# Optimization experiments

Hardware: AMD Instinct MI355X
Metric: run time of the kernel (lower is better)

Reference implementation:

```python
import jax, jax.numpy as jnp
import numpy as np

N_GROUPS = 32
EPS = 1e-5
N_HEADS = 8
D_K = 64


def setup_inputs() -> dict:
    key = jax.random.key(0)
    ks = jax.random.split(key, 4)
    B, C, H, W = 16, 512, 32, 32
    x = jax.random.normal(ks[0], (B, C, H, W), dtype=jnp.float32)
    gn_w = jnp.ones((C,), dtype=jnp.float32)
    gn_b = jnp.zeros((C,), dtype=jnp.float32)
    proj_w = jax.random.normal(ks[1], (3 * C, C), dtype=jnp.float32) * (C ** -0.5)
    proj_b = jnp.zeros((3 * C,), dtype=jnp.float32)
    out_w = jax.random.normal(ks[2], (C, C), dtype=jnp.float32) * (C ** -0.5)
    out_b = jnp.zeros((C,), dtype=jnp.float32)
    return {"x": x, "gn_w": gn_w, "gn_b": gn_b, "proj_w": proj_w,
            "proj_b": proj_b, "out_w": out_w, "out_b": out_b}


def _group_norm(x, w, b):
    B, C, H, W = x.shape
    xg = x.reshape(B, N_GROUPS, C // N_GROUPS, H, W)
    mean = xg.mean(axis=(2, 3, 4), keepdims=True)
    var = xg.var(axis=(2, 3, 4), keepdims=True)
    xn = (xg - mean) * jax.lax.rsqrt(var + EPS)
    xn = xn.reshape(B, C, H, W)
    return xn * w[None, :, None, None] + b[None, :, None, None]


def reference(x, gn_w, gn_b, proj_w, proj_b, out_w, out_b):
    B, C, H, W = x.shape
    S = H * W
    scale = D_K ** -0.25  # applied to both q and k, as in the original
    h = _group_norm(x, gn_w, gn_b).reshape(B, C, S).transpose(0, 2, 1)  # [B,S,C]
    qkv = h @ proj_w.T + proj_b  # [B,S,3C]
    qkv = qkv.reshape(B, S, N_HEADS, 3 * D_K)
    q, k, v = jnp.split(qkv, 3, axis=-1)  # each [B,S,H,D]
    attn = jnp.einsum('bihd,bjhd->bijh', q * scale, k * scale)  # [B,S,S,Hd]
    attn = jax.nn.softmax(attn, axis=2)
    res = jnp.einsum('bijh,bjhd->bihd', attn, v).reshape(B, S, N_HEADS * D_K)
    res = res @ out_w.T + out_b  # [B,S,C]
    res = res.transpose(0, 2, 1).reshape(B, C, H, W)
    return res + x
```

## Files before the change

### kernel.cpp

```cpp
#include <hip/hip_runtime.h>
#include <stdint.h>

typedef unsigned short u16;
typedef __attribute__((ext_vector_type(8))) short bf16x8;
typedef __attribute__((ext_vector_type(4))) short bf16x4;
typedef __attribute__((ext_vector_type(4))) float f32x4;
typedef __attribute__((ext_vector_type(4))) unsigned short u16x4;

#define GLD16(gp, lp) __builtin_amdgcn_global_load_lds( \
    (__attribute__((address_space(1))) void*)(void*)(gp), \
    (__attribute__((address_space(3))) void*)(void*)(lp), 16, 0, 0)

__device__ __forceinline__ u16 f2b(float f) {
  union { float f; unsigned u; } v; v.f = f;
  unsigned r = v.u + 0x7FFFu + ((v.u >> 16) & 1u);
  return (u16)(r >> 16);
}

__device__ __forceinline__ float fexp2(float x) {
#if __has_builtin(__builtin_amdgcn_exp2f)
  return __builtin_amdgcn_exp2f(x);
#else
  return exp2f(x);
#endif
}

__global__ __launch_bounds__(256) void cvt_kernel(const float* __restrict__ wq_f,
                                                  const float* __restrict__ wo_f,
                                                  u16* __restrict__ wq,
                                                  u16* __restrict__ wo) {
  int i = blockIdx.x * 256 + threadIdx.x;
  const float* src; u16* dst; int j;
  if (i < 196608) { src = wq_f; dst = wq; j = i; }
  else            { src = wo_f; dst = wo; j = i - 196608; }
  const float4 f = ((const float4*)src)[j];
  u16x4 r; r[0] = f2b(f.x); r[1] = f2b(f.y); r[2] = f2b(f.z); r[3] = f2b(f.w);
  *(u16x4*)(dst + (size_t)j * 4) = r;
}

__global__ __launch_bounds__(256) void gn_kernel(const float* __restrict__ x,
                                                 const float* __restrict__ gw,
                                                 const float* __restrict__ gb,
                                                 u16* __restrict__ h) {
  const int b = blockIdx.x >> 5, g = blockIdx.x & 31;
  const float* xg = x + ((size_t)(b * 512 + g * 16)) * 1024;
  const int tid = threadIdx.x;
  float vals[64];
  float s = 0.f, ss = 0.f;
#pragma unroll
  for (int i = 0; i < 64; i++) {
    float vv = xg[i * 256 + tid];
    vals[i] = vv; s += vv; ss += vv * vv;
  }
#pragma unroll
  for (int off = 32; off; off >>= 1) { s += __shfl_down(s, off); ss += __shfl_down(ss, off); }
  __shared__ float red[8];
  const int wid = tid >> 6, lane = tid & 63;
  if (lane == 0) { red[wid] = s; red[4 + wid] = ss; }
  __syncthreads();
  if (tid == 0) {
    float S = red[0] + red[1] + red[2] + red[3];
    float SS = red[4] + red[5] + red[6] + red[7];
    float mean = S * (1.f / 16384.f);
    float var = SS * (1.f / 16384.f) - mean * mean;
    red[0] = mean; red[1] = rsqrtf(var + 1e-5f);
  }
  __syncthreads();
  const float mean = red[0], rs = red[1];
  float sc[16], bi[16];
#pragma unroll
  for (int c = 0; c < 16; c++) { sc[c] = gw[g * 16 + c] * rs; bi[c] = gb[g * 16 + c]; }
#pragma unroll
  for (int h4 = 0; h4 < 4; h4++) {
    const int sp = h4 * 256 + tid;
    u16 row[16];
#pragma unroll
    for (int c = 0; c < 16; c++)
      row[c] = f2b((vals[c * 4 + h4] - mean) * sc[c] + bi[c]);
    u16* dst = h + ((size_t)(b * 1024 + sp)) * 512 + g * 16;
    *(bf16x8*)dst = *(bf16x8*)&row[0];
    *(bf16x8*)(dst + 8) = *(bf16x8*)&row[8];
  }
}

__global__ __launch_bounds__(256) void qkv_gemm(const u16* __restrict__ h,
                                                const u16* __restrict__ w,
                                                const float* __restrict__ bias,
                                                u16* __restrict__ q,
                                                u16* __restrict__ k,
                                                u16* __restrict__ v) {
  __shared__ u16 As[128 * 32];
  __shared__ u16 Bs[128 * 32];
  const int b = blockIdx.z;
  const int bm = blockIdx.x;
  const int bn = blockIdx.y;
  const int tid = threadIdx.x, lane = tid & 63, wid = tid >> 6;
  const int wm = wid & 1, wn = wid >> 1;
  const u16* gA = h + ((size_t)b * 1024 + bm * 128) * 512;
  const u16* gB = w + (size_t)bn * 128 * 512;

  const f32x4 fz = {0.f, 0.f, 0.f, 0.f};
  f32x4 acc[4][4];
#pragma unroll
  for (int i = 0; i < 4; i++)
#pragma unroll
    for (int j = 0; j < 4; j++) acc[i][j] = fz;

  const int r0 = lane >> 2;
  const int ch8 = (lane & 3) * 8;

  for (int kt = 0; kt < 16; ++kt) {
    __syncthreads();
#pragma unroll
    for (int j = 0; j < 2; ++j) {
      const int idx = wid * 2 + j;
      const int row = idx * 16 + r0;
      GLD16(gA + (size_t)row * 512 + kt * 32 + ch8, &As[idx * 512 + lane * 8]);
      GLD16(gB + (size_t)row * 512 + kt * 32 + ch8, &Bs[idx * 512 + lane * 8]);
    }
    __syncthreads();
    bf16x8 af[4], bf[4];
#pragma unroll
    for (int mi = 0; mi < 4; mi++)
      af[mi] = *(const bf16x8*)&As[(wm * 64 + mi * 16 + (lane & 15)) * 32 + (lane >> 4) * 8];
#pragma unroll
    for (int ni = 0; ni < 4; ni++)
      bf[ni] = *(const bf16x8*)&Bs[(wn * 64 + ni * 16 + (lane & 15)) * 32 + (lane >> 4) * 8];
#pragma unroll
    for (int mi = 0; mi < 4; mi++)
#pragma unroll
      for (int ni = 0; ni < 4; ni++)
        acc[mi][ni] = __builtin_amdgcn_mfma_f32_16x16x32_bf16(af[mi], bf[ni], acc[mi][ni], 0, 0, 0);
  }

  const float qscale = 0.51006972f;
  const float kscale = 0.35355339059327373f;
  const int quad4 = (lane >> 4) << 2;
#pragma unroll
  for (int mi = 0; mi < 4; mi++) {
    const int m = bm * 128 + wm * 64 + mi * 16 + quad4;
#pragma unroll
    for (int ni = 0; ni < 4; ni++) {
      const int n = bn * 128 + wn * 64 + ni * 16 + (lane & 15);
      const int head = n / 192;
      const int rr = n - head * 192;
      const float bi = bias[n];
      const int d = rr & 63;
      if (rr < 128) {
        u16* dst = (rr < 64) ? q : k;
        const float sc = (rr < 64) ? qscale : kscale;
        dst += ((size_t)(b * 8 + head) * 1024 + m) * 64 + d;
#pragma unroll
        for (int r = 0; r < 4; r++)
          dst[(size_t)r * 64] = f2b((acc[mi][ni][r] + bi) * sc);
      } else {
        u16x4 pk;
#pragma unroll
        for (int r = 0; r < 4; r++) pk[r] = f2b(acc[mi][ni][r] + bi);
        *(u16x4*)(v + ((size_t)(b * 8 + head) * 64 + d) * 1024 + m) = pk;
      }
    }
  }
}

__global__ __launch_bounds__(512) void attn_kernel(const u16* __restrict__ q,
                                                   const u16* __restrict__ k,
                                                   const u16* __restrict__ vT,
                                                   u16* __restrict__ o) {
  __shared__ u16 Ks[2][64 * 64];
  __shared__ u16 Vs[2][64 * 64];
  const int bh = blockIdx.x;
  const int qb = blockIdx.y;
  const int tid = threadIdx.x, lane = tid & 63, wid = tid >> 6;
  const u16* Q = q + (size_t)bh * 1024 * 64;
  const u16* K = k + (size_t)bh * 1024 * 64;
  const u16* V = vT + (size_t)bh * 64 * 1024;
  const int qrow0 = qb * 256 + wid * 32;
  const int c15 = lane & 15, quad = lane >> 4;
  const int sw = c15 & 7;
  const int srow = tid >> 3;
  const int u8g  = tid & 7;
  const int s7 = srow & 7;
  const int kld = srow * 64 + ((u8g ^ s7) * 8);
  const int ve = 4 * (u8g >> 2) + 2 * (u8g & 1);
  const int vc = ((u8g >> 1) & 1) * 4;
  const int vld0 = srow * 64 + ((ve ^ s7) * 8) + vc;
  const int vld1 = srow * 64 + (((ve + 1) ^ s7) * 8) + vc;

  bf16x8 qf[2][2];
#pragma unroll
  for (int kk = 0; kk < 2; kk++)
#pragma unroll
    for (int ni = 0; ni < 2; ni++)
      qf[kk][ni] = *(const bf16x8*)(Q + (size_t)(qrow0 + ni * 16 + c15) * 64 + kk * 32 + quad * 8);

  const f32x4 fz = {0.f, 0.f, 0.f, 0.f};
  const float Mshift = 14.4269504089f;
  const f32x4 fm = {-Mshift, -Mshift, -Mshift, -Mshift};
  f32x4 oaccT[4][2];
#pragma unroll
  for (int i = 0; i < 4; i++)
#pragma unroll
    for (int j = 0; j < 2; j++) oaccT[i][j] = fz;
  float lsum[2] = {0.f, 0.f};

  bf16x8 kr, vr;
  kr = *(const bf16x8*)(K + (size_t)srow * 64 + u8g * 8);
  vr = *(const bf16x8*)(V + (size_t)srow * 1024 + u8g * 8);
  {
    u16* Kd = Ks[0]; u16* Vd = Vs[0];
    *(bf16x8*)&Kd[kld] = kr;
    union { bf16x4 h[2]; bf16x8 v; } a; a.v = vr;
    *(bf16x4*)&Vd[vld0] = a.h[0];
    *(bf16x4*)&Vd[vld1] = a.h[1];
  }
  kr = *(const bf16x8*)(K + (size_t)(64 + srow) * 64 + u8g * 8);
  vr = *(const bf16x8*)(V + (size_t)srow * 1024 + 64 + u8g * 8);

  for (int kt = 0; kt < 16; ++kt) {
    __syncthreads();
    const int cur = kt & 1, alt = cur ^ 1;
    if (kt < 15) {
      u16* Kd = Ks[alt]; u16* Vd = Vs[alt];
      *(bf16x8*)&Kd[kld] = kr;
      union { bf16x4 h[2]; bf16x8 v; } a; a.v = vr;
      *(bf16x4*)&Vd[vld0] = a.h[0];
      *(bf16x4*)&Vd[vld1] = a.h[1];
      const int pk2 = (kt + 2) & 15;
      kr = *(const bf16x8*)(K + ((size_t)pk2 * 64 + srow) * 64 + u8g * 8);
      vr = *(const bf16x8*)(V + (size_t)srow * 1024 + pk2 * 64 + u8g * 8);
    }
    const u16* Kc = Ks[cur];
    const u16* Vc = Vs[cur];

    f32x4 sacc[4][2];
#pragma unroll
    for (int i = 0; i < 4; i++)
#pragma unroll
      for (int j = 0; j < 2; j++) sacc[i][j] = fm;
#pragma unroll
    for (int kk = 0; kk < 2; kk++) {
      bf16x8 af[4];
#pragma unroll
      for (int mi = 0; mi < 4; mi++)
        af[mi] = *(const bf16x8*)&Kc[(mi * 16 + c15) * 64 + (((kk * 4 + quad) ^ sw) * 8)];
      __builtin_amdgcn_s_setprio(1);
#pragma unroll
      for (int mi = 0; mi < 4; mi++)
#pragma unroll
        for (int ni = 0; ni < 2; ni++)
          sacc[mi][ni] = __builtin_amdgcn_mfma_f32_16x16x32_bf16(af[mi], qf[kk][ni], sacc[mi][ni], 0, 0, 0);
      __builtin_amdgcn_s_setprio(0);
    }

    unsigned pkd[4][2][2];
#pragma unroll
    for (int ni = 0; ni < 2; ni++) {
      float ls = 0.f;
#pragma unroll
      for (int mi = 0; mi < 4; mi++) {
        unsigned pu[4];
#pragma unroll
        for (int r = 0; r < 4; r++) {
          const float p = fexp2(sacc[mi][ni][r]);
          ls += p;
          union { float f; unsigned u; } c; c.f = p;
          pu[r] = c.u;
        }
        pkd[mi][ni][0] = __builtin_amdgcn_perm(pu[1], pu[0], 0x07060302u);
        pkd[mi][ni][1] = __builtin_amdgcn_perm(pu[3], pu[2], 0x07060302u);
      }
      lsum[ni] += ls;
    }

#pragma unroll
    for (int mg = 0; mg < 2; mg++) {
      union { unsigned u[4]; bf16x8 v; } bb[2];
#pragma unroll
      for (int ni = 0; ni < 2; ni++) {
        bb[ni].u[0] = pkd[2 * mg][ni][0];     bb[ni].u[1] = pkd[2 * mg][ni][1];
        bb[ni].u[2] = pkd[2 * mg + 1][ni][0]; bb[ni].u[3] = pkd[2 * mg + 1][ni][1];
      }
      bf16x8 aa[4];
#pragma unroll
      for (int nd = 0; nd < 4; nd++)
        aa[nd] = *(const bf16x8*)&Vc[(nd * 16 + c15) * 64 + (((mg * 4 + quad) ^ sw) * 8)];
      __builtin_amdgcn_s_setprio(1);
#pragma unroll
      for (int nd = 0; nd < 4; nd++)
#pragma unroll
        for (int ni = 0; ni < 2; ni++)
          oaccT[nd][ni] = __builtin_amdgcn_mfma_f32_16x16x32_bf16(aa[nd], bb[ni].v, oaccT[nd][ni], 0, 0, 0);
      __builtin_amdgcn_s_setprio(0);
    }
  }

  float iv[2];
#pragma unroll
  for (int ni = 0; ni < 2; ni++) {
    float l = lsum[ni];
    l += __shfl_xor(l, 16);
    l += __shfl_xor(l, 32);
    iv[ni] = 1.f / l;
  }
  const int b = bh >> 3, hh = bh & 7;
#pragma unroll
  for (int ni = 0; ni < 2; ni++) {
    const int row = qrow0 + ni * 16 + c15;
#pragma unroll
    for (int nd = 0; nd < 4; nd++) {
      u16x4 pk4;
#pragma unroll
      for (int r = 0; r < 4; r++) pk4[r] = f2b(oaccT[nd][ni][r] * iv[ni]);
      *(u16x4*)(o + ((size_t)b * 1024 + row) * 512 + hh * 64 + nd * 16 + quad * 4) = pk4;
    }
  }
}

__global__ __launch_bounds__(256) void out_gemm(const u16* __restrict__ wo,
                                                const u16* __restrict__ attn,
                                                const float* __restrict__ ob,
                                                const float* __restrict__ x,
                                                float* __restrict__ out) {
  __shared__ u16 As[128 * 32];
  __shared__ u16 Bs[128 * 32];
  const int b = blockIdx.z;
  const int bm = blockIdx.x;
  const int bn = blockIdx.y;
  const int tid = threadIdx.x, lane = tid & 63, wid = tid >> 6;
  const int wm = wid & 1, wn = wid >> 1;
  const u16* gA = wo + (size_t)bm * 128 * 512;
  const u16* gB = attn + ((size_t)b * 1024 + bn * 128) * 512;

  const f32x4 fz = {0.f, 0.f, 0.f, 0.f};
  f32x4 acc[4][4];
#pragma unroll
  for (int i = 0; i < 4; i++)
#pragma unroll
    for (int j = 0; j < 4; j++) acc[i][j] = fz;

  const int r0 = lane >> 2;
  const int ch8 = (lane & 3) * 8;

  for (int kt = 0; kt < 16; ++kt) {
    __syncthreads();
#pragma unroll
    for (int j = 0; j < 2; ++j) {
      const int idx = wid * 2 + j;
      const int row = idx * 16 + r0;
      GLD16(gA + (size_t)row * 512 + kt * 32 + ch8, &As[idx * 512 + lane * 8]);
      GLD16(gB + (size_t)row * 512 + kt * 32 + ch8, &Bs[idx * 512 + lane * 8]);
    }
    __syncthreads();
    bf16x8 af[4], bf[4];
#pragma unroll
    for (int mi = 0; mi < 4; mi++)
      af[mi] = *(const bf16x8*)&As[(wm * 64 + mi * 16 + (lane & 15)) * 32 + (lane >> 4) * 8];
#pragma unroll
    for (int ni = 0; ni < 4; ni++)
      bf[ni] = *(const bf16x8*)&Bs[(wn * 64 + ni * 16 + (lane & 15)) * 32 + (lane >> 4) * 8];
#pragma unroll
    for (int mi = 0; mi < 4; mi++)
#pragma unroll
      for (int ni = 0; ni < 4; ni++)
        acc[mi][ni] = __builtin_amdgcn_mfma_f32_16x16x32_bf16(af[mi], bf[ni], acc[mi][ni], 0, 0, 0);
  }

  const int quad4 = (lane >> 4) << 2;
#pragma unroll
  for (int mi = 0; mi < 4; mi++) {
    const int c = bm * 128 + wm * 64 + mi * 16 + quad4;
#pragma unroll
    for (int ni = 0; ni < 4; ni++) {
      const int s = bn * 128 + wn * 64 + ni * 16 + (lane & 15);
#pragma unroll
      for (int r = 0; r < 4; r++) {
        const int cc = c + r;
        const size_t idx = ((size_t)b * 512 + cc) * 1024 + s;
        out[idx] = acc[mi][ni][r] + ob[cc] + x[idx];
      }
    }
  }
}

extern "C" void kernel_launch(void* const* d_in, const int* in_sizes, int n_in,
                              void* d_out, int out_size, void* d_ws, size_t ws_size,
                              hipStream_t stream) {
  const float* x      = (const float*)d_in[0];
  const float* gn_w   = (const float*)d_in[1];
  const float* gn_b   = (const float*)d_in[2];
  const float* proj_w = (const float*)d_in[3];
  const float* proj_b = (const float*)d_in[4];
  const float* out_w  = (const float*)d_in[5];
  const float* out_b  = (const float*)d_in[6];
  float* out = (float*)d_out;

  char* p = (char*)d_ws;
  u16* h    = (u16*)p; p += (size_t)16 * 1024 * 512 * 2;
  u16* q    = (u16*)p; p += (size_t)16 * 8 * 1024 * 64 * 2;
  u16* k    = (u16*)p; p += (size_t)16 * 8 * 1024 * 64 * 2;
  u16* v    = (u16*)p; p += (size_t)16 * 8 * 1024 * 64 * 2;
  u16* attn = (u16*)p; p += (size_t)16 * 1024 * 512 * 2;
  u16* wq   = (u16*)p; p += (size_t)1536 * 512 * 2;
  u16* wo   = (u16*)p; p += (size_t)512 * 512 * 2;

  cvt_kernel<<<1024, 256, 0, stream>>>(proj_w, out_w, wq, wo);
  gn_kernel<<<512, 256, 0, stream>>>(x, gn_w, gn_b, h);
  qkv_gemm<<<dim3(8, 12, 16), 256, 0, stream>>>(h, wq, proj_b, q, k, v);
  attn_kernel<<<dim3(128, 4), 512, 0, stream>>>(q, k, v, attn);
  out_gemm<<<dim3(4, 8, 16), 256, 0, stream>>>(wo, attn, out_b, x, out);
}
```

Measured before the change: 207.9 us.

## Restructure QKV GEMM with double-buffered swizzled LDS and larger tiles

The QKV projection GEMM is rewritten to use 256x128 tiles with 512 threads, a K-step of 64, double-buffered LDS filled by direct global-to-LDS loads, and an XOR swizzle on LDS columns to avoid bank conflicts. The batch dimension is folded into M. MFMA phases are interleaved with fragment loads under explicit barriers and raised wave priority. The aim is to overlap global loads with compute and raise reuse per LDS byte. The cost is higher LDS use (96KB per block) and fewer blocks per CU.

```diff
diff --git a/kernel.cpp b/kernel.cpp
--- a/kernel.cpp
+++ b/kernel.cpp
@@ -83,21 +83,28 @@
   }
 }
 
-__global__ __launch_bounds__(256) void qkv_gemm(const u16* __restrict__ h,
-                                                const u16* __restrict__ w,
-                                                const float* __restrict__ bias,
-                                                u16* __restrict__ q,
-                                                u16* __restrict__ k,
-                                                u16* __restrict__ v) {
-  __shared__ u16 As[128 * 32];
-  __shared__ u16 Bs[128 * 32];
-  const int b = blockIdx.z;
+__global__ __launch_bounds__(512, 2) void qkv_gemm(const u16* __restrict__ h,
+                                                   const u16* __restrict__ w,
+                                                   const float* __restrict__ bias,
+                                                   u16* __restrict__ q,
+                                                   u16* __restrict__ k,
+                                                   u16* __restrict__ v) {
+  __shared__ u16 As[2][256 * 64];
+  __shared__ u16 Bs[2][128 * 64];
   const int bm = blockIdx.x;
   const int bn = blockIdx.y;
   const int tid = threadIdx.x, lane = tid & 63, wid = tid >> 6;
-  const int wm = wid & 1, wn = wid >> 1;
-  const u16* gA = h + ((size_t)b * 1024 + bm * 128) * 512;
+  const int wm = wid >> 1, wn = wid & 1;
+  const int c15 = lane & 15, quad = lane >> 4;
+  const int sw = c15 & 7;
+  const u16* gA = h + (size_t)bm * 256 * 512;
   const u16* gB = w + (size_t)bn * 128 * 512;
+
+  const int sr = tid >> 3;
+  const int lch = (tid & 7) ^ (sr & 7);
+  const u16* sA = gA + (size_t)sr * 512 + lch * 8;
+  const u16* sB = gB + (size_t)sr * 512 + lch * 8;
+  const int sdst = tid * 8;
 
   const f32x4 fz = {0.f, 0.f, 0.f, 0.f};
   f32x4 acc[4][4];
@@ -106,42 +113,84 @@
 #pragma unroll
     for (int j = 0; j < 4; j++) acc[i][j] = fz;
 
-  const int r0 = lane >> 2;
-  const int ch8 = (lane & 3) * 8;
-
-  for (int kt = 0; kt < 16; ++kt) {
-    __syncthreads();
-#pragma unroll
-    for (int j = 0; j < 2; ++j) {
-      const int idx = wid * 2 + j;
-      const int row = idx * 16 + r0;
-      GLD16(gA + (size_t)row * 512 + kt * 32 + ch8, &As[idx * 512 + lane * 8]);
-      GLD16(gB + (size_t)row * 512 + kt * 32 + ch8, &Bs[idx * 512 + lane * 8]);
-    }
-    __syncthreads();
-    bf16x8 af[4], bf[4];
-#pragma unroll
-    for (int mi = 0; mi < 4; mi++)
-      af[mi] = *(const bf16x8*)&As[(wm * 64 + mi * 16 + (lane & 15)) * 32 + (lane >> 4) * 8];
-#pragma unroll
-    for (int ni = 0; ni < 4; ni++)
-      bf[ni] = *(const bf16x8*)&Bs[(wn * 64 + ni * 16 + (lane & 15)) * 32 + (lane >> 4) * 8];
-#pragma unroll
-    for (int mi = 0; mi < 4; mi++)
-#pragma unroll
-      for (int ni = 0; ni < 4; ni++)
-        acc[mi][ni] = __builtin_amdgcn_mfma_f32_16x16x32_bf16(af[mi], bf[ni], acc[mi][ni], 0, 0, 0);
+#pragma unroll
+  for (int r = 0; r < 4; r++)
+    GLD16(sA + (size_t)r * 32768, &As[0][r * 4096 + sdst]);
+#pragma unroll
+  for (int r = 0; r < 2; r++)
+    GLD16(sB + (size_t)r * 32768, &Bs[0][r * 4096 + sdst]);
+  asm volatile("s_waitcnt vmcnt(0)" ::: "memory");
+  __builtin_amdgcn_s_barrier();
+  __builtin_amdgcn_sched_barrier(0);
+
+  for (int kt = 0; kt < 8; ++kt) {
+    const int c = kt & 1, d = c ^ 1;
+    if (kt < 7) {
+      const size_t ko = (size_t)(kt + 1) * 64;
+#pragma unroll
+      for (int r = 0; r < 4; r++)
+        GLD16(sA + (size_t)r * 32768 + ko, &As[d][r * 4096 + sdst]);
+#pragma unroll
+      for (int r = 0; r < 2; r++)
+        GLD16(sB + (size_t)r * 32768 + ko, &Bs[d][r * 4096 + sdst]);
+    }
+    bf16x8 af[2][4], bfx[2][2];
+#pragma unroll
+    for (int kk = 0; kk < 2; kk++) {
+      const int kc = ((kk * 4 + quad) ^ sw) * 8;
+#pragma unroll
+      for (int mi = 0; mi < 4; mi++)
+        af[kk][mi] = *(const bf16x8*)&As[c][(wm * 64 + mi * 16 + c15) * 64 + kc];
+#pragma unroll
+      for (int ni = 0; ni < 2; ni++)
+        bfx[kk][ni] = *(const bf16x8*)&Bs[c][(wn * 64 + ni * 16 + c15) * 64 + kc];
+    }
+    __builtin_amdgcn_s_barrier();
+    __builtin_amdgcn_sched_barrier(0);
+    __builtin_amdgcn_s_setprio(1);
+#pragma unroll
+    for (int kk = 0; kk < 2; kk++)
+#pragma unroll
+      for (int mi = 0; mi < 4; mi++)
+#pragma unroll
+        for (int ni = 0; ni < 2; ni++)
+          acc[mi][ni] = __builtin_amdgcn_mfma_f32_16x16x32_bf16(af[kk][mi], bfx[kk][ni], acc[mi][ni], 0, 0, 0);
+    __builtin_amdgcn_s_setprio(0);
+    __builtin_amdgcn_s_barrier();
+    __builtin_amdgcn_sched_barrier(0);
+#pragma unroll
+    for (int kk = 0; kk < 2; kk++) {
+      const int kc = ((kk * 4 + quad) ^ sw) * 8;
+#pragma unroll
+      for (int ni = 0; ni < 2; ni++)
+        bfx[kk][ni] = *(const bf16x8*)&Bs[c][(wn * 64 + (2 + ni) * 16 + c15) * 64 + kc];
+    }
+    __builtin_amdgcn_s_barrier();
+    __builtin_amdgcn_sched_barrier(0);
+    __builtin_amdgcn_s_setprio(1);
+#pragma unroll
+    for (int kk = 0; kk < 2; kk++)
+#pragma unroll
+      for (int mi = 0; mi < 4; mi++)
+#pragma unroll
+        for (int ni = 0; ni < 2; ni++)
+          acc[mi][2 + ni] = __builtin_amdgcn_mfma_f32_16x16x32_bf16(af[kk][mi], bfx[kk][ni], acc[mi][2 + ni], 0, 0, 0);
+    __builtin_amdgcn_s_setprio(0);
+    if (kt < 7) asm volatile("s_waitcnt vmcnt(0)" ::: "memory");
+    __builtin_amdgcn_s_barrier();
+    __builtin_amdgcn_sched_barrier(0);
   }
 
   const float qscale = 0.51006972f;
   const float kscale = 0.35355339059327373f;
-  const int quad4 = (lane >> 4) << 2;
+  const int quad4 = quad << 2;
 #pragma unroll
   for (int mi = 0; mi < 4; mi++) {
-    const int m = bm * 128 + wm * 64 + mi * 16 + quad4;
+    const int m = bm * 256 + wm * 64 + mi * 16 + quad4;
+    const int b = m >> 10, sp = m & 1023;
 #pragma unroll
     for (int ni = 0; ni < 4; ni++) {
-      const int n = bn * 128 + wn * 64 + ni * 16 + (lane & 15);
+      const int n = bn * 128 + wn * 64 + ni * 16 + c15;
       const int head = n / 192;
       const int rr = n - head * 192;
       const float bi = bias[n];
@@ -149,7 +198,7 @@
       if (rr < 128) {
         u16* dst = (rr < 64) ? q : k;
         const float sc = (rr < 64) ? qscale : kscale;
-        dst += ((size_t)(b * 8 + head) * 1024 + m) * 64 + d;
+        dst += ((size_t)(b * 8 + head) * 1024 + sp) * 64 + d;
 #pragma unroll
         for (int r = 0; r < 4; r++)
           dst[(size_t)r * 64] = f2b((acc[mi][ni][r] + bi) * sc);
@@ -157,7 +206,7 @@
         u16x4 pk;
 #pragma unroll
         for (int r = 0; r < 4; r++) pk[r] = f2b(acc[mi][ni][r] + bi);
-        *(u16x4*)(v + ((size_t)(b * 8 + head) * 64 + d) * 1024 + m) = pk;
+        *(u16x4*)(v + ((size_t)(b * 8 + head) * 64 + d) * 1024 + sp) = pk;
       }
     }
   }
@@ -406,7 +455,7 @@
 
   cvt_kernel<<<1024, 256, 0, stream>>>(proj_w, out_w, wq, wo);
   gn_kernel<<<512, 256, 0, stream>>>(x, gn_w, gn_b, h);
-  qkv_gemm<<<dim3(8, 12, 16), 256, 0, stream>>>(h, wq, proj_b, q, k, v);
+  qkv_gemm<<<dim3(64, 12), 512, 0, stream>>>(h, wq, proj_b, q, k, v);
   attn_kernel<<<dim3(128, 4), 512, 0, stream>>>(q, k, v, attn);
   out_gemm<<<dim3(4, 8, 16), 256, 0, stream>>>(wo, attn, out_b, x, out);
 }
```

Result: no change. 207.8 us (-0.1%).

## Vectorize GroupNorm loads via group-strip h layout and swap out_gemm operands

Applied to the files above, without the earlier changes.

GroupNorm now reads x with float4 loads and writes the normalized activations in a group-strip layout ([b][group][spatial][16]) as contiguous 32-byte runs per thread, instead of scattered 32-byte writes at a 1 KB stride. qkv_gemm's A-tile loader is rewritten to address this strip layout. out_gemm swaps its operands so the accumulator's four per-lane values fall on consecutive spatial positions, which allows float4 loads of the residual x and float4 stores of the output. The change aims to cut uncoalesced global traffic in GroupNorm and in the output epilogue, at the cost of a less contiguous A-tile gather in qkv_gemm.

```diff
diff --git a/kernel.cpp b/kernel.cpp
--- a/kernel.cpp
+++ b/kernel.cpp
@@ -45,12 +45,14 @@
   const int b = blockIdx.x >> 5, g = blockIdx.x & 31;
   const float* xg = x + ((size_t)(b * 512 + g * 16)) * 1024;
   const int tid = threadIdx.x;
-  float vals[64];
+  float4 vals[16];
   float s = 0.f, ss = 0.f;
 #pragma unroll
-  for (int i = 0; i < 64; i++) {
-    float vv = xg[i * 256 + tid];
-    vals[i] = vv; s += vv; ss += vv * vv;
+  for (int j = 0; j < 16; j++) {
+    const float4 v = ((const float4*)xg)[j * 256 + tid];
+    vals[j] = v;
+    s  += (v.x + v.y) + (v.z + v.w);
+    ss += (v.x * v.x + v.y * v.y) + (v.z * v.z + v.w * v.w);
   }
 #pragma unroll
   for (int off = 32; off; off >>= 1) { s += __shfl_down(s, off); ss += __shfl_down(ss, off); }
@@ -70,16 +72,17 @@
   float sc[16], bi[16];
 #pragma unroll
   for (int c = 0; c < 16; c++) { sc[c] = gw[g * 16 + c] * rs; bi[c] = gb[g * 16 + c]; }
-#pragma unroll
-  for (int h4 = 0; h4 < 4; h4++) {
-    const int sp = h4 * 256 + tid;
+  u16* dst = h + ((size_t)(b * 32 + g) * 1024 + 4 * tid) * 16;
+#pragma unroll
+  for (int e = 0; e < 4; e++) {
     u16 row[16];
 #pragma unroll
-    for (int c = 0; c < 16; c++)
-      row[c] = f2b((vals[c * 4 + h4] - mean) * sc[c] + bi[c]);
-    u16* dst = h + ((size_t)(b * 1024 + sp)) * 512 + g * 16;
-    *(bf16x8*)dst = *(bf16x8*)&row[0];
-    *(bf16x8*)(dst + 8) = *(bf16x8*)&row[8];
+    for (int j = 0; j < 16; j++) {
+      const float v = (e == 0) ? vals[j].x : (e == 1) ? vals[j].y : (e == 2) ? vals[j].z : vals[j].w;
+      row[j] = f2b((v - mean) * sc[j] + bi[j]);
+    }
+    *(bf16x8*)(dst + e * 16) = *(bf16x8*)&row[0];
+    *(bf16x8*)(dst + e * 16 + 8) = *(bf16x8*)&row[8];
   }
 }
 
@@ -96,7 +99,7 @@
   const int bn = blockIdx.y;
   const int tid = threadIdx.x, lane = tid & 63, wid = tid >> 6;
   const int wm = wid & 1, wn = wid >> 1;
-  const u16* gA = h + ((size_t)b * 1024 + bm * 128) * 512;
+  const u16* gA = h + (size_t)b * 524288 + (size_t)bm * 128 * 16;
   const u16* gB = w + (size_t)bn * 128 * 512;
 
   const f32x4 fz = {0.f, 0.f, 0.f, 0.f};
@@ -111,11 +114,13 @@
 
   for (int kt = 0; kt < 16; ++kt) {
     __syncthreads();
+    const int chA = kt * 32 + ch8;
+    const int gstrip = chA >> 4, rem = chA & 15;
 #pragma unroll
     for (int j = 0; j < 2; ++j) {
       const int idx = wid * 2 + j;
       const int row = idx * 16 + r0;
-      GLD16(gA + (size_t)row * 512 + kt * 32 + ch8, &As[idx * 512 + lane * 8]);
+      GLD16(gA + (size_t)gstrip * 16384 + (size_t)row * 16 + rem, &As[idx * 512 + lane * 8]);
       GLD16(gB + (size_t)row * 512 + kt * 32 + ch8, &Bs[idx * 512 + lane * 8]);
     }
     __syncthreads();
@@ -317,8 +322,8 @@
   }
 }
 
-__global__ __launch_bounds__(256) void out_gemm(const u16* __restrict__ wo,
-                                                const u16* __restrict__ attn,
+__global__ __launch_bounds__(256) void out_gemm(const u16* __restrict__ attn,
+                                                const u16* __restrict__ wo,
                                                 const float* __restrict__ ob,
                                                 const float* __restrict__ x,
                                                 float* __restrict__ out) {
@@ -329,8 +334,8 @@
   const int bn = blockIdx.y;
   const int tid = threadIdx.x, lane = tid & 63, wid = tid >> 6;
   const int wm = wid & 1, wn = wid >> 1;
-  const u16* gA = wo + (size_t)bm * 128 * 512;
-  const u16* gB = attn + ((size_t)b * 1024 + bn * 128) * 512;
+  const u16* gA = attn + ((size_t)b * 1024 + bm * 128) * 512;
+  const u16* gB = wo + (size_t)bn * 128 * 512;
 
   const f32x4 fz = {0.f, 0.f, 0.f, 0.f};
   f32x4 acc[4][4];
@@ -367,18 +372,22 @@
   }
 
   const int quad4 = (lane >> 4) << 2;
+  const int c15_ = lane & 15;
 #pragma unroll
   for (int mi = 0; mi < 4; mi++) {
-    const int c = bm * 128 + wm * 64 + mi * 16 + quad4;
+    const int m = bm * 128 + wm * 64 + mi * 16 + quad4;
 #pragma unroll
     for (int ni = 0; ni < 4; ni++) {
-      const int s = bn * 128 + wn * 64 + ni * 16 + (lane & 15);
-#pragma unroll
-      for (int r = 0; r < 4; r++) {
-        const int cc = c + r;
-        const size_t idx = ((size_t)b * 512 + cc) * 1024 + s;
-        out[idx] = acc[mi][ni][r] + ob[cc] + x[idx];
-      }
+      const int c = bn * 128 + wn * 64 + ni * 16 + c15_;
+      const float bo = ob[c];
+      const size_t idx = ((size_t)b * 512 + c) * 1024 + m;
+      const float4 xv = *(const float4*)(x + idx);
+      float4 ov;
+      ov.x = acc[mi][ni][0] + bo + xv.x;
+      ov.y = acc[mi][ni][1] + bo + xv.y;
+      ov.z = acc[mi][ni][2] + bo + xv.z;
+      ov.w = acc[mi][ni][3] + bo + xv.w;
+      *(float4*)(out + idx) = ov;
     }
   }
 }
@@ -408,5 +417,5 @@
   gn_kernel<<<512, 256, 0, stream>>>(x, gn_w, gn_b, h);
   qkv_gemm<<<dim3(8, 12, 16), 256, 0, stream>>>(h, wq, proj_b, q, k, v);
   attn_kernel<<<dim3(128, 4), 512, 0, stream>>>(q, k, v, attn);
-  out_gemm<<<dim3(4, 8, 16), 256, 0, stream>>>(wo, attn, out_b, x, out);
-}
+  out_gemm<<<dim3(8, 4, 16), 256, 0, stream>>>(attn, wo, out_b, x, out);
+}
```

New measurement: 210.4 us. No clear change (+1.2%).
